# Performance work log

Measured on AMD Instinct MI355X. Metric: run time of the kernel, lower is better.

Reference implementation:

```python
import jax, jax.numpy as jnp
import numpy as np

B, S, D, H = 2, 2048, 2048, 16
HD = D // H
EPS = 1e-5


def layernorm(x, scale, shift):
    mean = jnp.mean(x, axis=-1, keepdims=True)
    var = jnp.mean((x - mean) ** 2, axis=-1, keepdims=True)  # unbiased=False
    return scale * (x - mean) / jnp.sqrt(var + EPS) + shift


def gelu_buggy(x):
    # Faithful to source: tanh is applied ONLY to the constant sqrt(2/pi)
    c = jnp.tanh(jnp.sqrt(jnp.asarray(2.0 / jnp.pi, dtype=x.dtype)))
    return 0.5 * x * (1.0 + c * (x + 0.044715 * x ** 3))


def setup_inputs() -> dict:
    key = jax.random.key(0)
    ks = jax.random.split(key, 10)
    sd = 0.02
    return {
        "x": jax.random.normal(ks[0], (B, S, D), dtype=jnp.float32),
        "wq": jax.random.normal(ks[1], (D, D), dtype=jnp.float32) * sd,
        "wk": jax.random.normal(ks[2], (D, D), dtype=jnp.float32) * sd,
        "wv": jax.random.normal(ks[3], (D, D), dtype=jnp.float32) * sd,
        "wo": jax.random.normal(ks[4], (D, D), dtype=jnp.float32) * sd,
        "bo": jnp.zeros((D,), dtype=jnp.float32),
        "w1": jax.random.normal(ks[5], (D, 4 * D), dtype=jnp.float32) * sd,
        "b1": jnp.zeros((4 * D,), dtype=jnp.float32),
        "w2": jax.random.normal(ks[6], (4 * D, D), dtype=jnp.float32) * sd,
        "b2": jnp.zeros((D,), dtype=jnp.float32),
        "ln_scale": jnp.ones((D,), dtype=jnp.float32),
        "ln_shift": jnp.zeros((D,), dtype=jnp.float32),
    }


def attention(h, wq, wk, wv, wo, bo):
    b, s, _ = h.shape
    q = (h @ wq).reshape(b, s, H, HD).transpose(0, 2, 1, 3)  # [b,h,s,hd]
    k = (h @ wk).reshape(b, s, H, HD).transpose(0, 2, 1, 3)
    v = (h @ wv).reshape(b, s, H, HD).transpose(0, 2, 1, 3)
    scores = jnp.einsum('bhqd,bhkd->bhqk', q, k)
    causal = jnp.tril(jnp.ones((s, s), dtype=bool))
    scores = jnp.where(causal, scores, -jnp.inf)
    w = jax.nn.softmax(scores / jnp.sqrt(jnp.asarray(HD, dtype=h.dtype)), axis=-1)
    ctx = jnp.einsum('bhqk,bhkd->bhqd', w, v).transpose(0, 2, 1, 3).reshape(b, s, D)
    return ctx @ wo + bo


def reference(x, wq, wk, wv, wo, bo, w1, b1, w2, b2, ln_scale, ln_shift):
    # NB: source applies ln1 before BOTH sub-blocks (ln2 unused); dropout is identity (p=0 / eval)
    shortcut = x
    h = layernorm(x, ln_scale, ln_shift)
    h = attention(h, wq, wk, wv, wo, bo)
    x = h + shortcut
    shortcut = x
    h = layernorm(x, ln_scale, ln_shift)
    h = gelu_buggy(h @ w1 + b1) @ w2 + b2
    return h + shortcut
```

## Files before the change

### kernel.cpp

```cpp
#include <hip/hip_runtime.h>
#include <hip/hip_bf16.h>
#include <math.h>


typedef short bf16x8 __attribute__((ext_vector_type(8)));
typedef float f32x4 __attribute__((ext_vector_type(4)));
typedef short short4v __attribute__((ext_vector_type(4)));

#define MFMA16x32(a, b, c) __builtin_amdgcn_mfma_f32_16x16x32_bf16((a), (b), (c), 0, 0, 0)

__device__ __forceinline__ short f2bs(float f) {
    unsigned u = __builtin_bit_cast(unsigned, f);
    unsigned r = (u + 0x7FFFu + ((u >> 16) & 1u)) >> 16;
    return (short)(unsigned short)r;
}

__device__ __forceinline__ float bs2f(short s) {
    unsigned u = ((unsigned)(unsigned short)s) << 16;
    return __builtin_bit_cast(float, u);
}

__device__ __forceinline__ void gload_lds16(const void* g, void* l) {
    __builtin_amdgcn_global_load_lds(
        (const __attribute__((address_space(1))) unsigned int*)g,
        (__attribute__((address_space(3))) unsigned int*)l, 16, 0, 0);
}

template <int N>
__device__ __forceinline__ void vmw() {
    if constexpr (N == 0) asm volatile("s_waitcnt vmcnt(0)" ::: "memory");
    else if constexpr (N == 3) asm volatile("s_waitcnt vmcnt(3)" ::: "memory");
    else if constexpr (N == 6) asm volatile("s_waitcnt vmcnt(6)" ::: "memory");
    else if constexpr (N == 12) asm volatile("s_waitcnt vmcnt(12)" ::: "memory");
}

__global__ __launch_bounds__(256) void transpose_all_kernel(
    const float* __restrict__ wq, const float* __restrict__ wk,
    const float* __restrict__ wv, const float* __restrict__ wo,
    const float* __restrict__ w1, const float* __restrict__ w2,
    short* __restrict__ wqkvT, short* __restrict__ woT,
    short* __restrict__ w1T, short* __restrict__ w2T) {
    const int D = 2048;
    __shared__ float tile[32][33];
    int blk = blockIdx.x;
    const float* in;
    short* out;
    int R, C, bx, by;
    if (blk < 16384) {
        int r = blk >> 12;
        in = (r == 0) ? wq : (r == 1) ? wk : (r == 2) ? wv : wo;
        out = (r < 3) ? (wqkvT + (size_t)r * D * D) : woT;
        R = D; C = D;
        int lb = blk & 4095; bx = lb & 63; by = lb >> 6;
    } else if (blk < 32768) {
        in = w1; out = w1T; R = D; C = 4 * D;
        int lb = blk - 16384; bx = lb & 255; by = lb >> 8;
    } else {
        in = w2; out = w2T; R = 4 * D; C = D;
        int lb = blk - 32768; bx = lb & 63; by = lb >> 6;
    }
    const int tx = threadIdx.x & 31;
    const int ty = threadIdx.x >> 5;
    const int c0 = bx * 32, r0 = by * 32;
#pragma unroll
    for (int i = 0; i < 4; ++i) {
        int r = ty + i * 8;
        tile[r][tx] = in[(size_t)(r0 + r) * C + c0 + tx];
    }
    __syncthreads();
#pragma unroll
    for (int i = 0; i < 4; ++i) {
        int r = ty + i * 8;
        out[(size_t)(c0 + r) * R + r0 + tx] = f2bs(tile[tx][r]);
    }
}

__global__ __launch_bounds__(256) void ln_kernel(const float* __restrict__ x,
                                                 const float* __restrict__ sc,
                                                 const float* __restrict__ sh,
                                                 short* __restrict__ out) {
    const int D = 2048;
    const int row = blockIdx.x;
    const int tid = threadIdx.x;
    __shared__ float red[4];
    const float4* xr = (const float4*)(x + (size_t)row * D);
    float4 v0 = xr[tid];
    float4 v1 = xr[tid + 256];
    float vals0[4] = {v0.x, v0.y, v0.z, v0.w};
    float vals1[4] = {v1.x, v1.y, v1.z, v1.w};

    float s = vals0[0] + vals0[1] + vals0[2] + vals0[3] + vals1[0] + vals1[1] + vals1[2] + vals1[3];
#pragma unroll
    for (int off = 32; off; off >>= 1) s += __shfl_xor(s, off);
    if ((tid & 63) == 0) red[tid >> 6] = s;
    __syncthreads();
    float mean = (red[0] + red[1] + red[2] + red[3]) * (1.0f / 2048.0f);
    __syncthreads();

    float q = 0.0f;
#pragma unroll
    for (int j = 0; j < 4; ++j) {
        float t0 = vals0[j] - mean;
        float t1 = vals1[j] - mean;
        q += t0 * t0 + t1 * t1;
    }
#pragma unroll
    for (int off = 32; off; off >>= 1) q += __shfl_xor(q, off);
    if ((tid & 63) == 0) red[tid >> 6] = q;
    __syncthreads();
    float var = (red[0] + red[1] + red[2] + red[3]) * (1.0f / 2048.0f);
    float inv = rsqrtf(var + 1e-5f);

    const int c0 = tid * 4;
    const int c1 = (tid + 256) * 4;
    short4v o0, o1;
#pragma unroll
    for (int j = 0; j < 4; ++j) {
        o0[j] = f2bs(sc[c0 + j] * ((vals0[j] - mean) * inv) + sh[c0 + j]);
        o1[j] = f2bs(sc[c1 + j] * ((vals1[j] - mean) * inv) + sh[c1 + j]);
    }
    *(short4v*)(out + (size_t)row * D + c0) = o0;
    *(short4v*)(out + (size_t)row * D + c1) = o1;
}

__global__ __launch_bounds__(256) void ln_bf16_kernel(const short* __restrict__ x,
                                                      const float* __restrict__ sc,
                                                      const float* __restrict__ sh,
                                                      short* __restrict__ out) {
    const int D = 2048;
    const int row = blockIdx.x;
    const int tid = threadIdx.x;
    __shared__ float red[4];
    bf16x8 v = *(const bf16x8*)(x + (size_t)row * D + tid * 8);
    float vals[8];
#pragma unroll
    for (int j = 0; j < 8; ++j) vals[j] = bs2f(v[j]);

    float s = 0.f;
#pragma unroll
    for (int j = 0; j < 8; ++j) s += vals[j];
#pragma unroll
    for (int off = 32; off; off >>= 1) s += __shfl_xor(s, off);
    if ((tid & 63) == 0) red[tid >> 6] = s;
    __syncthreads();
    float mean = (red[0] + red[1] + red[2] + red[3]) * (1.0f / 2048.0f);
    __syncthreads();

    float q = 0.0f;
#pragma unroll
    for (int j = 0; j < 8; ++j) {
        float t = vals[j] - mean;
        q += t * t;
    }
#pragma unroll
    for (int off = 32; off; off >>= 1) q += __shfl_xor(q, off);
    if ((tid & 63) == 0) red[tid >> 6] = q;
    __syncthreads();
    float var = (red[0] + red[1] + red[2] + red[3]) * (1.0f / 2048.0f);
    float inv = rsqrtf(var + 1e-5f);

    const int c0 = tid * 8;
    bf16x8 o;
#pragma unroll
    for (int j = 0; j < 8; ++j)
        o[j] = f2bs(sc[c0 + j] * ((vals[j] - mean) * inv) + sh[c0 + j]);
    *(bf16x8*)(out + (size_t)row * D + c0) = o;
}

template <int EPI>
__global__ __launch_bounds__(512, 1) void gemm3d(const short* __restrict__ A,
                                                 const short* __restrict__ Bt,
                                                 int M, int N, int K,
                                                 void* __restrict__ Cout,
                                                 const float* __restrict__ bias,
                                                 const float* __restrict__ res,
                                                 float gconst) {
    extern __shared__ __align__(16) short lds[];
    const int tid = threadIdx.x;
    const int lane = tid & 63;
    const int wid = tid >> 6;
    const int wm = wid >> 1, wn = wid & 1;
    const int l15 = lane & 15, grp = lane >> 4;

    const int gx = gridDim.x;
    int flat = (int)blockIdx.y * gx + (int)blockIdx.x;
    const int cpx = (gx * (int)gridDim.y) >> 3;
    flat = (flat & 7) * cpx + (flat >> 3);
    const int bx = flat % gx, by = flat / gx;
    const long m0 = (long)by * 256, n0 = (long)bx * 128;

    f32x4 zero = {0.f, 0.f, 0.f, 0.f};
    f32x4 acc[4][4];
#pragma unroll
    for (int i = 0; i < 4; i++)
#pragma unroll
        for (int j = 0; j < 4; j++) acc[i][j] = zero;

    auto STAGE = [&](long k0, int b) {
        short* bufA = lds + b * 24576;
        short* bufB = bufA + 16384;
#pragma unroll
        for (int j = 0; j < 4; ++j) {
            int c = tid + j * 512;
            int row = c >> 3, sl = (c & 7) ^ (row & 7);
            gload_lds16(A + (size_t)(m0 + row) * K + k0 + sl * 8,
                        bufA + (size_t)(wid * 64 + j * 512) * 8);
        }
#pragma unroll
        for (int j = 0; j < 2; ++j) {
            int c = tid + j * 512;
            int row = c >> 3, sl = (c & 7) ^ (row & 7);
            gload_lds16(Bt + (size_t)(n0 + row) * K + k0 + sl * 8,
                        bufB + (size_t)(wid * 64 + j * 512) * 8);
        }
    };

    const int nt = K >> 6;
    STAGE(0, 0);
    STAGE(64, 1);
    int cur = 0, nx2 = 2;

    for (int t = 0; t < nt; ++t) {
        if (t + 2 < nt) {
            STAGE((long)(t + 2) * 64, nx2);
            vmw<12>();
        } else if (t + 1 < nt) {
            vmw<6>();
        } else {
            vmw<0>();
        }
        __builtin_amdgcn_s_barrier();
        __builtin_amdgcn_sched_barrier(0);

        const short* bufA = lds + cur * 24576;
        const short* bufB = bufA + 16384;
        bf16x8 af[2][4], bfr[2][4];
#pragma unroll
        for (int kk = 0; kk < 2; ++kk) {
#pragma unroll
            for (int m = 0; m < 4; ++m) {
                int row = wm * 64 + m * 16 + l15;
                af[kk][m] = *(const bf16x8*)(bufA + row * 64 + (((kk * 4 + grp) ^ (row & 7)) * 8));
            }
#pragma unroll
            for (int n = 0; n < 4; ++n) {
                int row = wn * 64 + n * 16 + l15;
                bfr[kk][n] = *(const bf16x8*)(bufB + row * 64 + (((kk * 4 + grp) ^ (row & 7)) * 8));
            }
        }
        __builtin_amdgcn_s_setprio(1);
#pragma unroll
        for (int kk = 0; kk < 2; ++kk)
#pragma unroll
            for (int m = 0; m < 4; ++m)
#pragma unroll
                for (int n = 0; n < 4; ++n)
                    acc[m][n] = MFMA16x32(af[kk][m], bfr[kk][n], acc[m][n]);
        __builtin_amdgcn_s_setprio(0);
        asm volatile("s_waitcnt lgkmcnt(0)" ::: "memory");
        __builtin_amdgcn_s_barrier();
        __builtin_amdgcn_sched_barrier(0);
        cur = (cur == 2) ? 0 : cur + 1;
        nx2 = (nx2 == 2) ? 0 : nx2 + 1;
    }

#pragma unroll
    for (int m = 0; m < 4; m++) {
        long gr = m0 + wm * 64 + m * 16 + grp * 4;
#pragma unroll
        for (int n = 0; n < 4; n++) {
            long gcol = n0 + wn * 64 + n * 16 + l15;
#pragma unroll
            for (int r = 0; r < 4; r++) {
                float vv = acc[m][n][r];
                long idx = (gr + r) * N + gcol;
                if constexpr (EPI == 0) {
                    ((short*)Cout)[idx] = f2bs(vv);
                } else if constexpr (EPI == 1) {
                    ((float*)Cout)[idx] = vv + bias[gcol] + res[idx];
                } else if constexpr (EPI == 2) {
                    float t2 = vv + bias[gcol];
                    float g = 0.5f * t2 * (1.0f + gconst * (t2 + 0.044715f * t2 * t2 * t2));
                    ((short*)Cout)[idx] = f2bs(g);
                } else if constexpr (EPI == 3) {
                    ((short*)Cout)[idx] = f2bs(vv + bias[gcol] + res[idx]);
                } else {
                    ((float*)Cout)[idx] = vv + bias[gcol] + bs2f(((const short*)res)[idx]);
                }
            }
        }
    }
}

template <int EPI>
__global__ __launch_bounds__(512, 4) void gemm3b(const short* __restrict__ A,
                                                 const short* __restrict__ Bt,
                                                 int M, int N, int K,
                                                 void* __restrict__ Cout,
                                                 const float* __restrict__ bias,
                                                 const float* __restrict__ res,
                                                 float gconst) {
    extern __shared__ __align__(16) short lds[];
    const int tid = threadIdx.x;
    const int lane = tid & 63;
    const int wid = tid >> 6;
    const int wm = wid >> 1, wn = wid & 1;
    const int l15 = lane & 15, grp = lane >> 4;

    const int gx = gridDim.x;
    int flat = (int)blockIdx.y * gx + (int)blockIdx.x;
    const int cpx = (gx * (int)gridDim.y) >> 3;
    flat = (flat & 7) * cpx + (flat >> 3);
    const int bx = flat % gx, by = flat / gx;
    const long m0 = (long)by * 256, n0 = (long)bx * 128;

    f32x4 zero = {0.f, 0.f, 0.f, 0.f};
    f32x4 acc[4][4];
#pragma unroll
    for (int i = 0; i < 4; i++)
#pragma unroll
        for (int j = 0; j < 4; j++) acc[i][j] = zero;

    auto STAGE = [&](int t, int b) {
        short* bufA = lds + b * 12288;
        short* bufB = bufA + 8192;
        const long k0 = (long)t << 5;
#pragma unroll
        for (int j = 0; j < 2; ++j) {
            int c = tid + j * 512;
            int row = c >> 2, sl = (c & 3) ^ ((row ^ (row >> 2)) & 3);
            gload_lds16(A + (size_t)(m0 + row) * K + k0 + sl * 8, bufA + (size_t)c * 8);
        }
        {
            int c = tid;
            int row = c >> 2, sl = (c & 3) ^ ((row ^ (row >> 2)) & 3);
            gload_lds16(Bt + (size_t)(n0 + row) * K + k0 + sl * 8, bufB + (size_t)c * 8);
        }
    };

    const int nt = K >> 5;
    STAGE(0, 0);
    STAGE(1, 1);
    int cur = 0, nx2 = 2;

    for (int t = 0; t < nt; ++t) {
        if (t + 2 < nt) {
            STAGE(t + 2, nx2);
            vmw<6>();
        } else if (t + 1 < nt) {
            vmw<3>();
        } else {
            vmw<0>();
        }
        __builtin_amdgcn_s_barrier();
        __builtin_amdgcn_sched_barrier(0);

        const short* bufA = lds + cur * 12288;
        const short* bufB = bufA + 8192;
        bf16x8 af[4], bfr[4];
#pragma unroll
        for (int m = 0; m < 4; ++m) {
            int row = wm * 64 + m * 16 + l15;
            af[m] = *(const bf16x8*)(bufA + row * 32 + (((grp ^ (row ^ (row >> 2))) & 3) * 8));
        }
#pragma unroll
        for (int n = 0; n < 4; ++n) {
            int row = wn * 64 + n * 16 + l15;
            bfr[n] = *(const bf16x8*)(bufB + row * 32 + (((grp ^ (row ^ (row >> 2))) & 3) * 8));
        }
        __builtin_amdgcn_s_setprio(1);
#pragma unroll
        for (int m = 0; m < 4; ++m)
#pragma unroll
            for (int n = 0; n < 4; ++n)
                acc[m][n] = MFMA16x32(af[m], bfr[n], acc[m][n]);
        __builtin_amdgcn_s_setprio(0);
        asm volatile("s_waitcnt lgkmcnt(0)" ::: "memory");
        __builtin_amdgcn_s_barrier();
        __builtin_amdgcn_sched_barrier(0);
        cur = (cur == 2) ? 0 : cur + 1;
        nx2 = (nx2 == 2) ? 0 : nx2 + 1;
    }

#pragma unroll
    for (int m = 0; m < 4; m++) {
        long gr = m0 + wm * 64 + m * 16 + grp * 4;
#pragma unroll
        for (int n = 0; n < 4; n++) {
            long gcol = n0 + wn * 64 + n * 16 + l15;
#pragma unroll
            for (int r = 0; r < 4; r++) {
                float vv = acc[m][n][r];
                long idx = (gr + r) * N + gcol;
                if constexpr (EPI == 0) {
                    ((short*)Cout)[idx] = f2bs(vv);
                } else if constexpr (EPI == 2) {
                    float t2 = vv + bias[gcol];
                    float g = 0.5f * t2 * (1.0f + gconst * (t2 + 0.044715f * t2 * t2 * t2));
                    ((short*)Cout)[idx] = f2bs(g);
                } else {
                    ((float*)Cout)[idx] = vv + bias[gcol] + res[idx];
                }
            }
        }
    }
}

__global__ __launch_bounds__(256) void reshape_v_kernel(const short* __restrict__ qkv,
                                                        short* __restrict__ Vt) {
    __shared__ short tile[32][33];
    const int bid = blockIdx.x;
    const int dt = bid & 3, st = (bid >> 2) & 63, bh = bid >> 8;
    const int b = bh >> 4, h = bh & 15;
    const int s0 = st * 32, d0 = dt * 32;
    const int tx = threadIdx.x & 31, ty = threadIdx.x >> 5;
#pragma unroll
    for (int i = 0; i < 4; ++i) {
        int s = ty + i * 8;
        tile[s][tx] = qkv[(size_t)(b * 2048 + s0 + s) * 6144 + 4096 + h * 128 + d0 + tx];
    }
    __syncthreads();
#pragma unroll
    for (int i = 0; i < 4; ++i) {
        int d = ty + i * 8;
        Vt[((size_t)bh * 128 + d0 + d) * 2048 + s0 + tx] = tile[tx][d];
    }
}

__global__ __launch_bounds__(256) void flash3_kernel(const short* __restrict__ qp,
                                                     const short* __restrict__ Vt,
                                                     short* __restrict__ ctx) {
    const int S = 2048, D = 2048, HD = 128, LD = 6144;
    __shared__ __align__(16) short Ks[2][64 * 128];
    __shared__ __align__(16) short Vs[2][64 * 128];
    __shared__ __align__(16) short Ps[4][16 * 64];
    const int tid = threadIdx.x;
    const int lane = tid & 63, wid = tid >> 6;
    const int l15 = lane & 15, grp = lane >> 4;

    int bid = (int)blockIdx.x;
    bid = (bid & 7) * 64 + (bid >> 3);
    const int p = bid & 15, bh = bid >> 4;
    const int b = bh >> 4, h = bh & 15;
    const int qtH = 31 - p;
    const int nH = qtH + 1;
    const float scale = 0.08838834764831845f;
    const float NEGINF = -__builtin_inff();

    const short* Kbase = qp + (size_t)b * S * LD + 2048 + (size_t)h * HD;
    const short* Vbase = Vt + (size_t)bh * 128 * S;
    short* Psw = &Ps[wid][0];

    f32x4 zero = {0.f, 0.f, 0.f, 0.f};
    bf16x8 aq[4];
    float m_[4], l_[4];
    f32x4 o[8];

    int qt = qtH;
    int qw = qt * 64 + wid * 16;
    {
        const short* qrow = qp + (size_t)(b * S + qw + l15) * LD + h * HD;
#pragma unroll
        for (int kc = 0; kc < 4; kc++) aq[kc] = *(const bf16x8*)(qrow + kc * 32 + grp * 8);
    }
#pragma unroll
    for (int r = 0; r < 4; r++) { m_[r] = NEGINF; l_[r] = 0.f; }
#pragma unroll
    for (int n = 0; n < 8; n++) o[n] = zero;

#pragma unroll
    for (int j = 0; j < 4; ++j) {
        int c = tid + j * 256;
        int r = c >> 4, sl = c & 15;
        gload_lds16(Kbase + (size_t)r * LD + ((sl ^ (r & 7)) * 8),
                    Ks[0] + (size_t)(wid * 64 + j * 256) * 8);
    }
#pragma unroll
    for (int j = 0; j < 4; ++j) {
        int c = tid + j * 256;
        int d = c >> 3, sl = c & 7;
        gload_lds16(Vbase + (size_t)d * S + ((sl ^ (d & 7)) * 8),
                    Vs[0] + (size_t)(wid * 64 + j * 256) * 8);
    }
    __syncthreads();

    int cur = 0;
    for (int i = 0; i < 33; ++i) {
        const int kt = (i < nH) ? i : (i - nH);
        const bool lastT = (kt == qt);

        if (i + 1 < 33) {
            const int ktn = (i + 1 < nH) ? (i + 1) : (i + 1 - nH);
            const long kn0 = (long)ktn * 64;
            const short* Kg = Kbase + (size_t)kn0 * LD;
            const short* Vg = Vbase + kn0;
            short* kd = Ks[cur ^ 1];
            short* vd = Vs[cur ^ 1];
#pragma unroll
            for (int j = 0; j < 4; ++j) {
                int c = tid + j * 256;
                int r = c >> 4, sl = c & 15;
                gload_lds16(Kg + (size_t)r * LD + ((sl ^ (r & 7)) * 8),
                            kd + (size_t)(wid * 64 + j * 256) * 8);
            }
#pragma unroll
            for (int j = 0; j < 4; ++j) {
                int c = tid + j * 256;
                int d = c >> 3, sl = c & 7;
                gload_lds16(Vg + (size_t)d * S + ((sl ^ (d & 7)) * 8),
                            vd + (size_t)(wid * 64 + j * 256) * 8);
            }
        }

        const short* Kc = Ks[cur];
        const short* Vc = Vs[cur];

        f32x4 s[4] = {zero, zero, zero, zero};
#pragma unroll
        for (int n = 0; n < 4; ++n) {
            int r = n * 16 + l15;
#pragma unroll
            for (int kc = 0; kc < 4; ++kc) {
                bf16x8 kb = *(const bf16x8*)(Kc + r * 128 + (((kc * 4 + grp) ^ (r & 7)) * 8));
                s[n] = MFMA16x32(aq[kc], kb, s[n]);
            }
        }

        float al[4];
#pragma unroll
        for (int r = 0; r < 4; ++r) {
            float v[4];
#pragma unroll
            for (int n = 0; n < 4; ++n) v[n] = s[n][r] * scale;
            if (lastT) {
                int qrel = wid * 16 + grp * 4 + r;
#pragma unroll
                for (int n = 0; n < 4; ++n)
                    if (n * 16 + l15 > qrel) v[n] = NEGINF;
            }
            float mx = fmaxf(fmaxf(v[0], v[1]), fmaxf(v[2], v[3]));
            mx = fmaxf(mx, __shfl_xor(mx, 1));
            mx = fmaxf(mx, __shfl_xor(mx, 2));
            mx = fmaxf(mx, __shfl_xor(mx, 4));
            mx = fmaxf(mx, __shfl_xor(mx, 8));
            float mn = fmaxf(m_[r], mx);
            float sc_ = __expf(m_[r] - mn);
            float rs = 0.f;
            int q = grp * 4 + r;
#pragma unroll
            for (int n = 0; n < 4; ++n) {
                v[n] = __expf(v[n] - mn);
                rs += v[n];
                Psw[q * 64 + (((n * 2 + (l15 >> 3)) ^ (q & 7)) * 8) + (l15 & 7)] = f2bs(v[n]);
            }
            rs += __shfl_xor(rs, 1);
            rs += __shfl_xor(rs, 2);
            rs += __shfl_xor(rs, 4);
            rs += __shfl_xor(rs, 8);
            l_[r] = l_[r] * sc_ + rs;
            m_[r] = mn;
            al[r] = sc_;
        }
#pragma unroll
        for (int n = 0; n < 8; n++) {
            f32x4 t = o[n];
            t[0] *= al[0]; t[1] *= al[1]; t[2] *= al[2]; t[3] *= al[3];
            o[n] = t;
        }

        bf16x8 pa[2];
#pragma unroll
        for (int kc = 0; kc < 2; ++kc)
            pa[kc] = *(const bf16x8*)(Psw + l15 * 64 + (((kc * 4 + grp) ^ (l15 & 7)) * 8));
#pragma unroll
        for (int n = 0; n < 8; ++n) {
            int d = n * 16 + l15;
#pragma unroll
            for (int kc = 0; kc < 2; ++kc) {
                bf16x8 vb = *(const bf16x8*)(Vc + d * 64 + (((kc * 4 + grp) ^ (d & 7)) * 8));
                o[n] = MFMA16x32(pa[kc], vb, o[n]);
            }
        }

        if (lastT) {
            float inv[4];
#pragma unroll
            for (int r = 0; r < 4; ++r) inv[r] = 1.0f / l_[r];
            short* cb_ = ctx + (size_t)(b * S + qw + grp * 4) * D + h * HD + l15;
#pragma unroll
            for (int n = 0; n < 8; ++n)
#pragma unroll
                for (int r = 0; r < 4; ++r)
                    cb_[(size_t)r * D + n * 16] = f2bs(o[n][r] * inv[r]);
            if (i < 32) {
                qt = 31 - qtH;
                qw = qt * 64 + wid * 16;
                const short* qrow = qp + (size_t)(b * S + qw + l15) * LD + h * HD;
#pragma unroll
                for (int kc = 0; kc < 4; kc++) aq[kc] = *(const bf16x8*)(qrow + kc * 32 + grp * 8);
#pragma unroll
                for (int r = 0; r < 4; r++) { m_[r] = NEGINF; l_[r] = 0.f; }
#pragma unroll
                for (int n = 0; n < 8; n++) o[n] = zero;
            }
        }
        __syncthreads();
        cur ^= 1;
    }
}

extern "C" void kernel_launch(void* const* d_in, const int* in_sizes, int n_in,
                              void* d_out, int out_size, void* d_ws, size_t ws_size,
                              hipStream_t stream) {
    const float* x    = (const float*)d_in[0];
    const float* wq   = (const float*)d_in[1];
    const float* wk   = (const float*)d_in[2];
    const float* wv   = (const float*)d_in[3];
    const float* wo   = (const float*)d_in[4];
    const float* bo   = (const float*)d_in[5];
    const float* w1   = (const float*)d_in[6];
    const float* b1   = (const float*)d_in[7];
    const float* w2   = (const float*)d_in[8];
    const float* b2   = (const float*)d_in[9];
    const float* lnsc = (const float*)d_in[10];
    const float* lnsh = (const float*)d_in[11];

    const int B = 2, S = 2048, D = 2048;
    const int M = B * S;
    const int LDS_3D = 3 * 24576 * 2;
    const int LDS_3B = 3 * 12288 * 2;

    char* p = (char*)d_ws;
    short* wqkvT = (short*)p; p += (size_t)3 * D * D * 2;
    short* woT   = (short*)p; p += (size_t)D * D * 2;
    short* w1T   = (short*)p; p += (size_t)4 * D * D * 2;
    short* w2T   = (short*)p; p += (size_t)4 * D * D * 2;
    short* lnb   = (short*)p; p += (size_t)M * D * 2;
    short* qkvb  = (short*)p;
    short* h1    = qkvb;
    p += (size_t)M * 3 * D * 2;
    short* ctxb  = (short*)p; p += (size_t)M * D * 2;
    short* x2    = (short*)p; p += (size_t)M * D * 2;

    short* Vt = x2;

    const float gconst = tanhf(sqrtf(2.0f / 3.14159265358979323846f));

    hipFuncSetAttribute((const void*)&gemm3d<0>, hipFuncAttributeMaxDynamicSharedMemorySize, LDS_3D);
    hipFuncSetAttribute((const void*)&gemm3d<3>, hipFuncAttributeMaxDynamicSharedMemorySize, LDS_3D);
    hipFuncSetAttribute((const void*)&gemm3d<4>, hipFuncAttributeMaxDynamicSharedMemorySize, LDS_3D);
    hipFuncSetAttribute((const void*)&gemm3b<2>, hipFuncAttributeMaxDynamicSharedMemorySize, LDS_3B);

    dim3 blk(256);
    transpose_all_kernel<<<dim3(49152), blk, 0, stream>>>(
        wq, wk, wv, wo, w1, w2, wqkvT, woT, w1T, w2T);

    ln_kernel<<<dim3(M), blk, 0, stream>>>(x, lnsc, lnsh, lnb);
    gemm3d<0><<<dim3(3 * D / 128, M / 256), dim3(512), LDS_3D, stream>>>(
        lnb, wqkvT, M, 3 * D, D, qkvb, nullptr, nullptr, 0.f);

    reshape_v_kernel<<<dim3(8192), blk, 0, stream>>>(qkvb, Vt);

    flash3_kernel<<<dim3(512), blk, 0, stream>>>(qkvb, Vt, ctxb);

    gemm3d<3><<<dim3(D / 128, M / 256), dim3(512), LDS_3D, stream>>>(
        ctxb, woT, M, D, D, x2, bo, x, 0.f);
    ln_bf16_kernel<<<dim3(M), blk, 0, stream>>>(x2, lnsc, lnsh, lnb);
    gemm3b<2><<<dim3(4 * D / 128, M / 256), dim3(512), LDS_3B, stream>>>(
        lnb, w1T, M, 4 * D, D, h1, b1, nullptr, gconst);
    gemm3d<4><<<dim3(D / 128, M / 256), dim3(512), LDS_3D, stream>>>(
        h1, w2T, M, D, 4 * D, (float*)d_out, b2, (const float*)x2, 0.f);
}
```

Measured before the change: 625.7 us.

## Use 128x128 double-buffered GEMM for the output projection and FC2

Adds a gemm2c kernel with 256 threads, 128x128 tiles, 64-wide K steps and a two-stage global-to-LDS double buffer. The Wo projection and FC2 GEMMs (N=2048) now use it instead of the 256x128 triple-buffered gemm3d. With 128-row tiles the grid has 512 workgroups instead of 256, which aims to fill the MI355X's compute units better on these narrower GEMMs. The cost is less data reuse per tile and a shallower pipeline that may hide less global-load latency.

```diff
diff --git a/kernel.cpp b/kernel.cpp
--- a/kernel.cpp
+++ b/kernel.cpp
@@ -31,6 +31,7 @@
     if constexpr (N == 0) asm volatile("s_waitcnt vmcnt(0)" ::: "memory");
     else if constexpr (N == 3) asm volatile("s_waitcnt vmcnt(3)" ::: "memory");
     else if constexpr (N == 6) asm volatile("s_waitcnt vmcnt(6)" ::: "memory");
+    else if constexpr (N == 8) asm volatile("s_waitcnt vmcnt(8)" ::: "memory");
     else if constexpr (N == 12) asm volatile("s_waitcnt vmcnt(12)" ::: "memory");
 }
 
@@ -293,6 +294,115 @@
 }
 
 template <int EPI>
+__global__ __launch_bounds__(256, 2) void gemm2c(const short* __restrict__ A,
+                                                 const short* __restrict__ Bt,
+                                                 int M, int N, int K,
+                                                 void* __restrict__ Cout,
+                                                 const float* __restrict__ bias,
+                                                 const float* __restrict__ res,
+                                                 float gconst) {
+    extern __shared__ __align__(16) short lds[];
+    const int tid = threadIdx.x;
+    const int lane = tid & 63;
+    const int wid = tid >> 6;
+    const int wm = wid >> 1, wn = wid & 1;
+    const int l15 = lane & 15, grp = lane >> 4;
+
+    const int gx = gridDim.x;
+    int flat = (int)blockIdx.y * gx + (int)blockIdx.x;
+    const int cpx = (gx * (int)gridDim.y) >> 3;
+    flat = (flat & 7) * cpx + (flat >> 3);
+    const int bx = flat % gx, by = flat / gx;
+    const long m0 = (long)by * 128, n0 = (long)bx * 128;
+
+    f32x4 zero = {0.f, 0.f, 0.f, 0.f};
+    f32x4 acc[4][4];
+#pragma unroll
+    for (int i = 0; i < 4; i++)
+#pragma unroll
+        for (int j = 0; j < 4; j++) acc[i][j] = zero;
+
+    auto STAGE = [&](int t, int b) {
+        short* bufA = lds + b * 16384;
+        short* bufB = bufA + 8192;
+        const long k0 = (long)t << 6;
+#pragma unroll
+        for (int j = 0; j < 4; ++j) {
+            int c = tid + j * 256;
+            int row = c >> 3, sl = (c & 7) ^ (row & 7);
+            gload_lds16(A + (size_t)(m0 + row) * K + k0 + sl * 8, bufA + (size_t)c * 8);
+        }
+#pragma unroll
+        for (int j = 0; j < 4; ++j) {
+            int c = tid + j * 256;
+            int row = c >> 3, sl = (c & 7) ^ (row & 7);
+            gload_lds16(Bt + (size_t)(n0 + row) * K + k0 + sl * 8, bufB + (size_t)c * 8);
+        }
+    };
+
+    const int nt = K >> 6;
+    STAGE(0, 0);
+    STAGE(1, 1);
+
+    for (int t = 0; t < nt; ++t) {
+        if (t + 1 < nt) { vmw<8>(); } else { vmw<0>(); }
+        __builtin_amdgcn_s_barrier();
+        __builtin_amdgcn_sched_barrier(0);
+
+        const short* bufA = lds + (t & 1) * 16384;
+        const short* bufB = bufA + 8192;
+        bf16x8 af[2][4], bfr[2][4];
+#pragma unroll
+        for (int kk = 0; kk < 2; ++kk) {
+#pragma unroll
+            for (int m = 0; m < 4; ++m) {
+                int row = wm * 64 + m * 16 + l15;
+                af[kk][m] = *(const bf16x8*)(bufA + row * 64 + (((kk * 4 + grp) ^ (row & 7)) * 8));
+            }
+#pragma unroll
+            for (int n = 0; n < 4; ++n) {
+                int row = wn * 64 + n * 16 + l15;
+                bfr[kk][n] = *(const bf16x8*)(bufB + row * 64 + (((kk * 4 + grp) ^ (row & 7)) * 8));
+            }
+        }
+        __builtin_amdgcn_s_setprio(1);
+#pragma unroll
+        for (int kk = 0; kk < 2; ++kk)
+#pragma unroll
+            for (int m = 0; m < 4; ++m)
+#pragma unroll
+                for (int n = 0; n < 4; ++n)
+                    acc[m][n] = MFMA16x32(af[kk][m], bfr[kk][n], acc[m][n]);
+        __builtin_amdgcn_s_setprio(0);
+        asm volatile("s_waitcnt lgkmcnt(0)" ::: "memory");
+        __builtin_amdgcn_s_barrier();
+        __builtin_amdgcn_sched_barrier(0);
+        if (t + 2 < nt) STAGE(t + 2, t & 1);
+    }
+
+#pragma unroll
+    for (int m = 0; m < 4; m++) {
+        long gr = m0 + wm * 64 + m * 16 + grp * 4;
+#pragma unroll
+        for (int n = 0; n < 4; n++) {
+            long gcol = n0 + wn * 64 + n * 16 + l15;
+#pragma unroll
+            for (int r = 0; r < 4; r++) {
+                float vv = acc[m][n][r];
+                long idx = (gr + r) * N + gcol;
+                if constexpr (EPI == 3) {
+                    ((short*)Cout)[idx] = f2bs(vv + bias[gcol] + res[idx]);
+                } else if constexpr (EPI == 4) {
+                    ((float*)Cout)[idx] = vv + bias[gcol] + bs2f(((const short*)res)[idx]);
+                } else {
+                    ((short*)Cout)[idx] = f2bs(vv);
+                }
+            }
+        }
+    }
+}
+
+template <int EPI>
 __global__ __launch_bounds__(512, 4) void gemm3b(const short* __restrict__ A,
                                                  const short* __restrict__ Bt,
                                                  int M, int N, int K,
@@ -629,6 +739,7 @@
     const int M = B * S;
     const int LDS_3D = 3 * 24576 * 2;
     const int LDS_3B = 3 * 12288 * 2;
+    const int LDS_2C = 2 * 16384 * 2;
 
     char* p = (char*)d_ws;
     short* wqkvT = (short*)p; p += (size_t)3 * D * D * 2;
@@ -647,9 +758,9 @@
     const float gconst = tanhf(sqrtf(2.0f / 3.14159265358979323846f));
 
     hipFuncSetAttribute((const void*)&gemm3d<0>, hipFuncAttributeMaxDynamicSharedMemorySize, LDS_3D);
-    hipFuncSetAttribute((const void*)&gemm3d<3>, hipFuncAttributeMaxDynamicSharedMemorySize, LDS_3D);
-    hipFuncSetAttribute((const void*)&gemm3d<4>, hipFuncAttributeMaxDynamicSharedMemorySize, LDS_3D);
     hipFuncSetAttribute((const void*)&gemm3b<2>, hipFuncAttributeMaxDynamicSharedMemorySize, LDS_3B);
+    hipFuncSetAttribute((const void*)&gemm2c<3>, hipFuncAttributeMaxDynamicSharedMemorySize, LDS_2C);
+    hipFuncSetAttribute((const void*)&gemm2c<4>, hipFuncAttributeMaxDynamicSharedMemorySize, LDS_2C);
 
     dim3 blk(256);
     transpose_all_kernel<<<dim3(49152), blk, 0, stream>>>(
@@ -663,11 +774,11 @@
 
     flash3_kernel<<<dim3(512), blk, 0, stream>>>(qkvb, Vt, ctxb);
 
-    gemm3d<3><<<dim3(D / 128, M / 256), dim3(512), LDS_3D, stream>>>(
+    gemm2c<3><<<dim3(D / 128, M / 128), blk, LDS_2C, stream>>>(
         ctxb, woT, M, D, D, x2, bo, x, 0.f);
     ln_bf16_kernel<<<dim3(M), blk, 0, stream>>>(x2, lnsc, lnsh, lnb);
     gemm3b<2><<<dim3(4 * D / 128, M / 256), dim3(512), LDS_3B, stream>>>(
         lnb, w1T, M, 4 * D, D, h1, b1, nullptr, gconst);
-    gemm3d<4><<<dim3(D / 128, M / 256), dim3(512), LDS_3D, stream>>>(
+    gemm2c<4><<<dim3(D / 128, M / 128), blk, LDS_2C, stream>>>(
         h1, w2T, M, D, 4 * D, (float*)d_out, b2, (const float*)x2, 0.f);
 }
```

New measurement: 598.5 us. -4.3%, faster.

## Replace GEMM kernels with 128x128-tile, 256-thread double-buffered GEMM

Applied to the files above, without the earlier changes.

Replaces both the 256x128 triple-buffered 512-thread GEMM and the BK=32 variant with a single 128x128 tile, 256-thread, two-stage double-buffered GEMM running two blocks per CU. The next stage is issued after the compute barrier instead of before the wait. The goal is more resident blocks and better latency hiding at lower LDS cost. In exchange each block reuses data less and the pipeline is shallower.

```diff
diff --git a/kernel.cpp b/kernel.cpp
--- a/kernel.cpp
+++ b/kernel.cpp
@@ -29,9 +29,7 @@
 template <int N>
 __device__ __forceinline__ void vmw() {
     if constexpr (N == 0) asm volatile("s_waitcnt vmcnt(0)" ::: "memory");
-    else if constexpr (N == 3) asm volatile("s_waitcnt vmcnt(3)" ::: "memory");
-    else if constexpr (N == 6) asm volatile("s_waitcnt vmcnt(6)" ::: "memory");
-    else if constexpr (N == 12) asm volatile("s_waitcnt vmcnt(12)" ::: "memory");
+    else if constexpr (N == 8) asm volatile("s_waitcnt vmcnt(8)" ::: "memory");
 }
 
 __global__ __launch_bounds__(256) void transpose_all_kernel(
@@ -168,7 +166,7 @@
 }
 
 template <int EPI>
-__global__ __launch_bounds__(512, 1) void gemm3d(const short* __restrict__ A,
+__global__ __launch_bounds__(256, 2) void gemm2c(const short* __restrict__ A,
                                                  const short* __restrict__ Bt,
                                                  int M, int N, int K,
                                                  void* __restrict__ Cout,
@@ -187,7 +185,7 @@
     const int cpx = (gx * (int)gridDim.y) >> 3;
     flat = (flat & 7) * cpx + (flat >> 3);
     const int bx = flat % gx, by = flat / gx;
-    const long m0 = (long)by * 256, n0 = (long)bx * 128;
+    const long m0 = (long)by * 128, n0 = (long)bx * 128;
 
     f32x4 zero = {0.f, 0.f, 0.f, 0.f};
     f32x4 acc[4][4];
@@ -196,44 +194,35 @@
 #pragma unroll
         for (int j = 0; j < 4; j++) acc[i][j] = zero;
 
-    auto STAGE = [&](long k0, int b) {
-        short* bufA = lds + b * 24576;
-        short* bufB = bufA + 16384;
+    auto STAGE = [&](int t, int b) {
+        short* bufA = lds + b * 16384;
+        short* bufB = bufA + 8192;
+        const long k0 = (long)t << 6;
 #pragma unroll
         for (int j = 0; j < 4; ++j) {
-            int c = tid + j * 512;
+            int c = tid + j * 256;
             int row = c >> 3, sl = (c & 7) ^ (row & 7);
-            gload_lds16(A + (size_t)(m0 + row) * K + k0 + sl * 8,
-                        bufA + (size_t)(wid * 64 + j * 512) * 8);
-        }
-#pragma unroll
-        for (int j = 0; j < 2; ++j) {
-            int c = tid + j * 512;
+            gload_lds16(A + (size_t)(m0 + row) * K + k0 + sl * 8, bufA + (size_t)c * 8);
+        }
+#pragma unroll
+        for (int j = 0; j < 4; ++j) {
+            int c = tid + j * 256;
             int row = c >> 3, sl = (c & 7) ^ (row & 7);
-            gload_lds16(Bt + (size_t)(n0 + row) * K + k0 + sl * 8,
-                        bufB + (size_t)(wid * 64 + j * 512) * 8);
+            gload_lds16(Bt + (size_t)(n0 + row) * K + k0 + sl * 8, bufB + (size_t)c * 8);
         }
     };
 
     const int nt = K >> 6;
     STAGE(0, 0);
-    STAGE(64, 1);
-    int cur = 0, nx2 = 2;
+    STAGE(1, 1);
 
     for (int t = 0; t < nt; ++t) {
-        if (t + 2 < nt) {
-            STAGE((long)(t + 2) * 64, nx2);
-            vmw<12>();
-        } else if (t + 1 < nt) {
-            vmw<6>();
-        } else {
-            vmw<0>();
-        }
+        if (t + 1 < nt) { vmw<8>(); } else { vmw<0>(); }
         __builtin_amdgcn_s_barrier();
         __builtin_amdgcn_sched_barrier(0);
 
-        const short* bufA = lds + cur * 24576;
-        const short* bufB = bufA + 16384;
+        const short* bufA = lds + (t & 1) * 16384;
+        const short* bufB = bufA + 8192;
         bf16x8 af[2][4], bfr[2][4];
 #pragma unroll
         for (int kk = 0; kk < 2; ++kk) {
@@ -260,126 +249,7 @@
         asm volatile("s_waitcnt lgkmcnt(0)" ::: "memory");
         __builtin_amdgcn_s_barrier();
         __builtin_amdgcn_sched_barrier(0);
-        cur = (cur == 2) ? 0 : cur + 1;
-        nx2 = (nx2 == 2) ? 0 : nx2 + 1;
-    }
-
-#pragma unroll
-    for (int m = 0; m < 4; m++) {
-        long gr = m0 + wm * 64 + m * 16 + grp * 4;
-#pragma unroll
-        for (int n = 0; n < 4; n++) {
-            long gcol = n0 + wn * 64 + n * 16 + l15;
-#pragma unroll
-            for (int r = 0; r < 4; r++) {
-                float vv = acc[m][n][r];
-                long idx = (gr + r) * N + gcol;
-                if constexpr (EPI == 0) {
-                    ((short*)Cout)[idx] = f2bs(vv);
-                } else if constexpr (EPI == 1) {
-                    ((float*)Cout)[idx] = vv + bias[gcol] + res[idx];
-                } else if constexpr (EPI == 2) {
-                    float t2 = vv + bias[gcol];
-                    float g = 0.5f * t2 * (1.0f + gconst * (t2 + 0.044715f * t2 * t2 * t2));
-                    ((short*)Cout)[idx] = f2bs(g);
-                } else if constexpr (EPI == 3) {
-                    ((short*)Cout)[idx] = f2bs(vv + bias[gcol] + res[idx]);
-                } else {
-                    ((float*)Cout)[idx] = vv + bias[gcol] + bs2f(((const short*)res)[idx]);
-                }
-            }
-        }
-    }
-}
-
-template <int EPI>
-__global__ __launch_bounds__(512, 4) void gemm3b(const short* __restrict__ A,
-                                                 const short* __restrict__ Bt,
-                                                 int M, int N, int K,
-                                                 void* __restrict__ Cout,
-                                                 const float* __restrict__ bias,
-                                                 const float* __restrict__ res,
-                                                 float gconst) {
-    extern __shared__ __align__(16) short lds[];
-    const int tid = threadIdx.x;
-    const int lane = tid & 63;
-    const int wid = tid >> 6;
-    const int wm = wid >> 1, wn = wid & 1;
-    const int l15 = lane & 15, grp = lane >> 4;
-
-    const int gx = gridDim.x;
-    int flat = (int)blockIdx.y * gx + (int)blockIdx.x;
-    const int cpx = (gx * (int)gridDim.y) >> 3;
-    flat = (flat & 7) * cpx + (flat >> 3);
-    const int bx = flat % gx, by = flat / gx;
-    const long m0 = (long)by * 256, n0 = (long)bx * 128;
-
-    f32x4 zero = {0.f, 0.f, 0.f, 0.f};
-    f32x4 acc[4][4];
-#pragma unroll
-    for (int i = 0; i < 4; i++)
-#pragma unroll
-        for (int j = 0; j < 4; j++) acc[i][j] = zero;
-
-    auto STAGE = [&](int t, int b) {
-        short* bufA = lds + b * 12288;
-        short* bufB = bufA + 8192;
-        const long k0 = (long)t << 5;
-#pragma unroll
-        for (int j = 0; j < 2; ++j) {
-            int c = tid + j * 512;
-            int row = c >> 2, sl = (c & 3) ^ ((row ^ (row >> 2)) & 3);
-            gload_lds16(A + (size_t)(m0 + row) * K + k0 + sl * 8, bufA + (size_t)c * 8);
-        }
-        {
-            int c = tid;
-            int row = c >> 2, sl = (c & 3) ^ ((row ^ (row >> 2)) & 3);
-            gload_lds16(Bt + (size_t)(n0 + row) * K + k0 + sl * 8, bufB + (size_t)c * 8);
-        }
-    };
-
-    const int nt = K >> 5;
-    STAGE(0, 0);
-    STAGE(1, 1);
-    int cur = 0, nx2 = 2;
-
-    for (int t = 0; t < nt; ++t) {
-        if (t + 2 < nt) {
-            STAGE(t + 2, nx2);
-            vmw<6>();
-        } else if (t + 1 < nt) {
-            vmw<3>();
-        } else {
-            vmw<0>();
-        }
-        __builtin_amdgcn_s_barrier();
-        __builtin_amdgcn_sched_barrier(0);
-
-        const short* bufA = lds + cur * 12288;
-        const short* bufB = bufA + 8192;
-        bf16x8 af[4], bfr[4];
-#pragma unroll
-        for (int m = 0; m < 4; ++m) {
-            int row = wm * 64 + m * 16 + l15;
-            af[m] = *(const bf16x8*)(bufA + row * 32 + (((grp ^ (row ^ (row >> 2))) & 3) * 8));
-        }
-#pragma unroll
-        for (int n = 0; n < 4; ++n) {
-            int row = wn * 64 + n * 16 + l15;
-            bfr[n] = *(const bf16x8*)(bufB + row * 32 + (((grp ^ (row ^ (row >> 2))) & 3) * 8));
-        }
-        __builtin_amdgcn_s_setprio(1);
-#pragma unroll
-        for (int m = 0; m < 4; ++m)
-#pragma unroll
-            for (int n = 0; n < 4; ++n)
-                acc[m][n] = MFMA16x32(af[m], bfr[n], acc[m][n]);
-        __builtin_amdgcn_s_setprio(0);
-        asm volatile("s_waitcnt lgkmcnt(0)" ::: "memory");
-        __builtin_amdgcn_s_barrier();
-        __builtin_amdgcn_sched_barrier(0);
-        cur = (cur == 2) ? 0 : cur + 1;
-        nx2 = (nx2 == 2) ? 0 : nx2 + 1;
+        if (t + 2 < nt) STAGE(t + 2, t & 1);
     }
 
 #pragma unroll
@@ -398,8 +268,10 @@
                     float t2 = vv + bias[gcol];
                     float g = 0.5f * t2 * (1.0f + gconst * (t2 + 0.044715f * t2 * t2 * t2));
                     ((short*)Cout)[idx] = f2bs(g);
+                } else if constexpr (EPI == 3) {
+                    ((short*)Cout)[idx] = f2bs(vv + bias[gcol] + res[idx]);
                 } else {
-                    ((float*)Cout)[idx] = vv + bias[gcol] + res[idx];
+                    ((float*)Cout)[idx] = vv + bias[gcol] + bs2f(((const short*)res)[idx]);
                 }
             }
         }
@@ -627,8 +499,7 @@
 
     const int B = 2, S = 2048, D = 2048;
     const int M = B * S;
-    const int LDS_3D = 3 * 24576 * 2;
-    const int LDS_3B = 3 * 12288 * 2;
+    const int LDS_2C = 2 * 16384 * 2;
 
     char* p = (char*)d_ws;
     short* wqkvT = (short*)p; p += (size_t)3 * D * D * 2;
@@ -646,28 +517,28 @@
 
     const float gconst = tanhf(sqrtf(2.0f / 3.14159265358979323846f));
 
-    hipFuncSetAttribute((const void*)&gemm3d<0>, hipFuncAttributeMaxDynamicSharedMemorySize, LDS_3D);
-    hipFuncSetAttribute((const void*)&gemm3d<3>, hipFuncAttributeMaxDynamicSharedMemorySize, LDS_3D);
-    hipFuncSetAttribute((const void*)&gemm3d<4>, hipFuncAttributeMaxDynamicSharedMemorySize, LDS_3D);
-    hipFuncSetAttribute((const void*)&gemm3b<2>, hipFuncAttributeMaxDynamicSharedMemorySize, LDS_3B);
+    hipFuncSetAttribute((const void*)&gemm2c<0>, hipFuncAttributeMaxDynamicSharedMemorySize, LDS_2C);
+    hipFuncSetAttribute((const void*)&gemm2c<2>, hipFuncAttributeMaxDynamicSharedMemorySize, LDS_2C);
+    hipFuncSetAttribute((const void*)&gemm2c<3>, hipFuncAttributeMaxDynamicSharedMemorySize, LDS_2C);
+    hipFuncSetAttribute((const void*)&gemm2c<4>, hipFuncAttributeMaxDynamicSharedMemorySize, LDS_2C);
 
     dim3 blk(256);
     transpose_all_kernel<<<dim3(49152), blk, 0, stream>>>(
         wq, wk, wv, wo, w1, w2, wqkvT, woT, w1T, w2T);
 
     ln_kernel<<<dim3(M), blk, 0, stream>>>(x, lnsc, lnsh, lnb);
-    gemm3d<0><<<dim3(3 * D / 128, M / 256), dim3(512), LDS_3D, stream>>>(
+    gemm2c<0><<<dim3(3 * D / 128, M / 128), blk, LDS_2C, stream>>>(
         lnb, wqkvT, M, 3 * D, D, qkvb, nullptr, nullptr, 0.f);
 
     reshape_v_kernel<<<dim3(8192), blk, 0, stream>>>(qkvb, Vt);
 
     flash3_kernel<<<dim3(512), blk, 0, stream>>>(qkvb, Vt, ctxb);
 
-    gemm3d<3><<<dim3(D / 128, M / 256), dim3(512), LDS_3D, stream>>>(
+    gemm2c<3><<<dim3(D / 128, M / 128), blk, LDS_2C, stream>>>(
         ctxb, woT, M, D, D, x2, bo, x, 0.f);
     ln_bf16_kernel<<<dim3(M), blk, 0, stream>>>(x2, lnsc, lnsh, lnb);
-    gemm3b<2><<<dim3(4 * D / 128, M / 256), dim3(512), LDS_3B, stream>>>(
+    gemm2c<2><<<dim3(4 * D / 128, M / 128), blk, LDS_2C, stream>>>(
         lnb, w1T, M, 4 * D, D, h1, b1, nullptr, gconst);
-    gemm3d<4><<<dim3(D / 128, M / 256), dim3(512), LDS_3D, stream>>>(
-        h1, w2T, M, D, 4 * D, (float*)d_out, b2, (const float*)x2, 0.f);
-}
+    gemm2c<4><<<dim3(D / 128, M / 128), blk, LDS_2C, stream>>>(
+        h1, w2T, M, D, 4 * D, (float*)d_out, b2, (const short*)x2 ? (const float*)x2 : nullptr, 0.f);
+}
```

New measurement: 629.7 us. No clear change (+0.6%).

## Replace three post-attention GEMMs with 128x128 BK64 double-buffered kernel

Applied to the files above, without the earlier changes.

Adds a new GEMM kernel with 256 threads, a 128x128 output tile and a K-step of 64. It double-buffers through LDS using an 8-way XOR swizzle, and issues the next stage's loads after the compute barrier. It also adds an optional column-major block swizzle, used for the FFN up-projection. This kernel replaces the 256x128 gemm3d/gemm3b variants for the output projection, FFN1 and FFN2, aiming at better occupancy, fewer barriers per K and better L2 locality. The trade-off is less reuse per block and a shallower prefetch (two stages instead of three).

```diff
diff --git a/kernel.cpp b/kernel.cpp
--- a/kernel.cpp
+++ b/kernel.cpp
@@ -29,8 +29,8 @@
 template <int N>
 __device__ __forceinline__ void vmw() {
     if constexpr (N == 0) asm volatile("s_waitcnt vmcnt(0)" ::: "memory");
-    else if constexpr (N == 3) asm volatile("s_waitcnt vmcnt(3)" ::: "memory");
     else if constexpr (N == 6) asm volatile("s_waitcnt vmcnt(6)" ::: "memory");
+    else if constexpr (N == 8) asm volatile("s_waitcnt vmcnt(8)" ::: "memory");
     else if constexpr (N == 12) asm volatile("s_waitcnt vmcnt(12)" ::: "memory");
 }
 
@@ -276,12 +276,6 @@
                 long idx = (gr + r) * N + gcol;
                 if constexpr (EPI == 0) {
                     ((short*)Cout)[idx] = f2bs(vv);
-                } else if constexpr (EPI == 1) {
-                    ((float*)Cout)[idx] = vv + bias[gcol] + res[idx];
-                } else if constexpr (EPI == 2) {
-                    float t2 = vv + bias[gcol];
-                    float g = 0.5f * t2 * (1.0f + gconst * (t2 + 0.044715f * t2 * t2 * t2));
-                    ((short*)Cout)[idx] = f2bs(g);
                 } else if constexpr (EPI == 3) {
                     ((short*)Cout)[idx] = f2bs(vv + bias[gcol] + res[idx]);
                 } else {
@@ -292,8 +286,8 @@
     }
 }
 
-template <int EPI>
-__global__ __launch_bounds__(512, 4) void gemm3b(const short* __restrict__ A,
+template <int EPI, bool CM>
+__global__ __launch_bounds__(256, 2) void gemm2c(const short* __restrict__ A,
                                                  const short* __restrict__ Bt,
                                                  int M, int N, int K,
                                                  void* __restrict__ Cout,
@@ -307,12 +301,14 @@
     const int wm = wid >> 1, wn = wid & 1;
     const int l15 = lane & 15, grp = lane >> 4;
 
-    const int gx = gridDim.x;
-    int flat = (int)blockIdx.y * gx + (int)blockIdx.x;
-    const int cpx = (gx * (int)gridDim.y) >> 3;
+    const int gx = gridDim.x, gy = gridDim.y;
+    int flat = CM ? ((int)blockIdx.x * gy + (int)blockIdx.y)
+                  : ((int)blockIdx.y * gx + (int)blockIdx.x);
+    const int cpx = (gx * gy) >> 3;
     flat = (flat & 7) * cpx + (flat >> 3);
-    const int bx = flat % gx, by = flat / gx;
-    const long m0 = (long)by * 256, n0 = (long)bx * 128;
+    const int bx = CM ? (flat / gy) : (flat % gx);
+    const int by = CM ? (flat % gy) : (flat / gx);
+    const long m0 = (long)by * 128, n0 = (long)bx * 128;
 
     f32x4 zero = {0.f, 0.f, 0.f, 0.f};
     f32x4 acc[4][4];
@@ -322,64 +318,61 @@
         for (int j = 0; j < 4; j++) acc[i][j] = zero;
 
     auto STAGE = [&](int t, int b) {
-        short* bufA = lds + b * 12288;
+        short* bufA = lds + b * 16384;
         short* bufB = bufA + 8192;
-        const long k0 = (long)t << 5;
-#pragma unroll
-        for (int j = 0; j < 2; ++j) {
-            int c = tid + j * 512;
-            int row = c >> 2, sl = (c & 3) ^ ((row ^ (row >> 2)) & 3);
+        const long k0 = (long)t << 6;
+#pragma unroll
+        for (int j = 0; j < 4; ++j) {
+            int c = tid + j * 256;
+            int row = c >> 3, sl = (c & 7) ^ (row & 7);
             gload_lds16(A + (size_t)(m0 + row) * K + k0 + sl * 8, bufA + (size_t)c * 8);
         }
-        {
-            int c = tid;
-            int row = c >> 2, sl = (c & 3) ^ ((row ^ (row >> 2)) & 3);
+#pragma unroll
+        for (int j = 0; j < 4; ++j) {
+            int c = tid + j * 256;
+            int row = c >> 3, sl = (c & 7) ^ (row & 7);
             gload_lds16(Bt + (size_t)(n0 + row) * K + k0 + sl * 8, bufB + (size_t)c * 8);
         }
     };
 
-    const int nt = K >> 5;
+    const int nt = K >> 6;
     STAGE(0, 0);
     STAGE(1, 1);
-    int cur = 0, nx2 = 2;
 
     for (int t = 0; t < nt; ++t) {
-        if (t + 2 < nt) {
-            STAGE(t + 2, nx2);
-            vmw<6>();
-        } else if (t + 1 < nt) {
-            vmw<3>();
-        } else {
-            vmw<0>();
-        }
+        if (t + 1 < nt) { vmw<8>(); } else { vmw<0>(); }
         __builtin_amdgcn_s_barrier();
         __builtin_amdgcn_sched_barrier(0);
 
-        const short* bufA = lds + cur * 12288;
+        const short* bufA = lds + (t & 1) * 16384;
         const short* bufB = bufA + 8192;
-        bf16x8 af[4], bfr[4];
-#pragma unroll
-        for (int m = 0; m < 4; ++m) {
-            int row = wm * 64 + m * 16 + l15;
-            af[m] = *(const bf16x8*)(bufA + row * 32 + (((grp ^ (row ^ (row >> 2))) & 3) * 8));
-        }
-#pragma unroll
-        for (int n = 0; n < 4; ++n) {
-            int row = wn * 64 + n * 16 + l15;
-            bfr[n] = *(const bf16x8*)(bufB + row * 32 + (((grp ^ (row ^ (row >> 2))) & 3) * 8));
+        bf16x8 af[2][4], bfr[2][4];
+#pragma unroll
+        for (int kk = 0; kk < 2; ++kk) {
+#pragma unroll
+            for (int m = 0; m < 4; ++m) {
+                int row = wm * 64 + m * 16 + l15;
+                af[kk][m] = *(const bf16x8*)(bufA + row * 64 + (((kk * 4 + grp) ^ (row & 7)) * 8));
+            }
+#pragma unroll
+            for (int n = 0; n < 4; ++n) {
+                int row = wn * 64 + n * 16 + l15;
+                bfr[kk][n] = *(const bf16x8*)(bufB + row * 64 + (((kk * 4 + grp) ^ (row & 7)) * 8));
+            }
         }
         __builtin_amdgcn_s_setprio(1);
 #pragma unroll
-        for (int m = 0; m < 4; ++m)
-#pragma unroll
-            for (int n = 0; n < 4; ++n)
-                acc[m][n] = MFMA16x32(af[m], bfr[n], acc[m][n]);
+        for (int kk = 0; kk < 2; ++kk)
+#pragma unroll
+            for (int m = 0; m < 4; ++m)
+#pragma unroll
+                for (int n = 0; n < 4; ++n)
+                    acc[m][n] = MFMA16x32(af[kk][m], bfr[kk][n], acc[m][n]);
         __builtin_amdgcn_s_setprio(0);
         asm volatile("s_waitcnt lgkmcnt(0)" ::: "memory");
         __builtin_amdgcn_s_barrier();
         __builtin_amdgcn_sched_barrier(0);
-        cur = (cur == 2) ? 0 : cur + 1;
-        nx2 = (nx2 == 2) ? 0 : nx2 + 1;
+        if (t + 2 < nt) STAGE(t + 2, t & 1);
     }
 
 #pragma unroll
@@ -392,14 +385,14 @@
             for (int r = 0; r < 4; r++) {
                 float vv = acc[m][n][r];
                 long idx = (gr + r) * N + gcol;
-                if constexpr (EPI == 0) {
-                    ((short*)Cout)[idx] = f2bs(vv);
-                } else if constexpr (EPI == 2) {
+                if constexpr (EPI == 2) {
                     float t2 = vv + bias[gcol];
                     float g = 0.5f * t2 * (1.0f + gconst * (t2 + 0.044715f * t2 * t2 * t2));
                     ((short*)Cout)[idx] = f2bs(g);
+                } else if constexpr (EPI == 3) {
+                    ((short*)Cout)[idx] = f2bs(vv + bias[gcol] + res[idx]);
                 } else {
-                    ((float*)Cout)[idx] = vv + bias[gcol] + res[idx];
+                    ((float*)Cout)[idx] = vv + bias[gcol] + bs2f(((const short*)res)[idx]);
                 }
             }
         }
@@ -628,7 +621,7 @@
     const int B = 2, S = 2048, D = 2048;
     const int M = B * S;
     const int LDS_3D = 3 * 24576 * 2;
-    const int LDS_3B = 3 * 12288 * 2;
+    const int LDS_2C = 2 * 16384 * 2;
 
     char* p = (char*)d_ws;
     short* wqkvT = (short*)p; p += (size_t)3 * D * D * 2;
@@ -647,9 +640,9 @@
     const float gconst = tanhf(sqrtf(2.0f / 3.14159265358979323846f));
 
     hipFuncSetAttribute((const void*)&gemm3d<0>, hipFuncAttributeMaxDynamicSharedMemorySize, LDS_3D);
-    hipFuncSetAttribute((const void*)&gemm3d<3>, hipFuncAttributeMaxDynamicSharedMemorySize, LDS_3D);
-    hipFuncSetAttribute((const void*)&gemm3d<4>, hipFuncAttributeMaxDynamicSharedMemorySize, LDS_3D);
-    hipFuncSetAttribute((const void*)&gemm3b<2>, hipFuncAttributeMaxDynamicSharedMemorySize, LDS_3B);
+    hipFuncSetAttribute((const void*)&gemm2c<2, true>, hipFuncAttributeMaxDynamicSharedMemorySize, LDS_2C);
+    hipFuncSetAttribute((const void*)&gemm2c<3, false>, hipFuncAttributeMaxDynamicSharedMemorySize, LDS_2C);
+    hipFuncSetAttribute((const void*)&gemm2c<4, false>, hipFuncAttributeMaxDynamicSharedMemorySize, LDS_2C);
 
     dim3 blk(256);
     transpose_all_kernel<<<dim3(49152), blk, 0, stream>>>(
@@ -663,11 +656,11 @@
 
     flash3_kernel<<<dim3(512), blk, 0, stream>>>(qkvb, Vt, ctxb);
 
-    gemm3d<3><<<dim3(D / 128, M / 256), dim3(512), LDS_3D, stream>>>(
+    gemm2c<3, false><<<dim3(D / 128, M / 128), blk, LDS_2C, stream>>>(
         ctxb, woT, M, D, D, x2, bo, x, 0.f);
     ln_bf16_kernel<<<dim3(M), blk, 0, stream>>>(x2, lnsc, lnsh, lnb);
-    gemm3b<2><<<dim3(4 * D / 128, M / 256), dim3(512), LDS_3B, stream>>>(
+    gemm2c<2, true><<<dim3(4 * D / 128, M / 128), blk, LDS_2C, stream>>>(
         lnb, w1T, M, 4 * D, D, h1, b1, nullptr, gconst);
-    gemm3d<4><<<dim3(D / 128, M / 256), dim3(512), LDS_3D, stream>>>(
+    gemm2c<4, false><<<dim3(D / 128, M / 128), blk, LDS_2C, stream>>>(
         h1, w2T, M, D, 4 * D, (float*)d_out, b2, (const float*)x2, 0.f);
 }
```

Result: no change. 622.1 us (-0.6%).
